# Performance work log

Hardware: AMD Instinct MI355X
Metric: run time of the kernel (lower is better)

Reference implementation:

```python
import jax, jax.numpy as jnp
import numpy as np

V, H, L, B, T = 50000, 256, 2, 4, 1024


def setup_inputs() -> dict:
    key = jax.random.key(0)
    ks = jax.random.split(key, 8)
    s = 1.0 / np.sqrt(H)
    return {
        "input_ids": jax.random.randint(ks[0], (B, T), 0, V),
        "emb": jax.random.normal(ks[1], (V, H), jnp.float32) * 0.02,
        "Wi": jax.random.normal(ks[2], (L, H, H), jnp.float32) * s,
        "bi": jnp.zeros((L, H), jnp.float32),
        "Wf": jax.random.normal(ks[3], (L, H, H), jnp.float32) * s,
        "bf": jnp.zeros((L, H), jnp.float32),
        "Wg": jax.random.normal(ks[4], (L, H, H), jnp.float32) * s,
        "bg": jnp.zeros((L, H), jnp.float32),
        "Wo": jax.random.normal(ks[5], (L, H, H), jnp.float32) * s,
        "bo": jnp.zeros((L, H), jnp.float32),
        "Wp": jax.random.normal(ks[6], (H, V), jnp.float32) * s,
        "bp": jnp.zeros((V,), jnp.float32),
    }


def _hgrn_layer(x, Wi_l, bi_l, Wf_l, bf_l, Wg_l, bg_l, Wo_l, bo_l, lower):
    # x: [B, T, H]
    i = jax.nn.silu(x @ Wi_l + bi_l)                              # input branch
    f = lower + (1.0 - lower) * jax.nn.sigmoid(x @ Wf_l + bf_l)   # bounded forget gate
    g = jax.nn.sigmoid(x @ Wg_l + bg_l)                           # output gate

    def step(h, fi):
        f_t, i_t = fi
        h = f_t * h + (1.0 - f_t) * i_t
        return h, h

    # scan over time: [T, B, H]
    h0 = jnp.zeros_like(x[:, 0])
    h_last, h_seq = jax.lax.scan(step, h0, (jnp.swapaxes(f, 0, 1), jnp.swapaxes(i, 0, 1)))
    h_seq = jnp.swapaxes(h_seq, 0, 1)                             # [B, T, H]
    out = (h_seq * g) @ Wo_l + bo_l
    return x + out, h_last


def reference(input_ids, emb, Wi, bi, Wf, bf, Wg, bg, Wo, bo, Wp, bp):
    x = emb[input_ids]                                            # [B, T, H]
    n_layers = Wi.shape[0]
    hiddens = []
    for l in range(n_layers):
        lower = l / n_layers
        x, h_last = _hgrn_layer(x, Wi[l], bi[l], Wf[l], bf[l], Wg[l], bg[l], Wo[l], bo[l], lower)
        hiddens.append(h_last)
    logits = x @ Wp + bp                                          # [B, T, V]
    return logits, jnp.stack(hiddens)                             # hidden: [L, B, H]
```

## Files before the change

### kernel.cpp

```cpp
#include <hip/hip_runtime.h>


#define VV 50000
#define HH 256
#define LL 2
#define BB 4
#define TT 1024
#define MM 4096
#define HID_OFF 204800000

typedef __attribute__((ext_vector_type(8))) short short8_t;
typedef __attribute__((ext_vector_type(4))) short short4_t;
typedef __attribute__((ext_vector_type(4))) float f32x4_t;

static __device__ __forceinline__ short f2bf(float f) {
  union { float f; unsigned u; } a;
  a.f = f;
  unsigned u = a.u;
  unsigned r = u + 0x7fffu + ((u >> 16) & 1u);
  return (short)(r >> 16);
}

__global__ __launch_bounds__(256) void k_embed(const int* __restrict__ ids,
                                               const float* __restrict__ emb,
                                               float* __restrict__ x,
                                               short* __restrict__ xb) {
  int row = blockIdx.x;
  int h = threadIdx.x;
  int id = ids[row];
  float v = emb[(size_t)id * HH + h];
  x[(size_t)row * HH + h] = v;
  xb[(size_t)row * HH + h] = f2bf(v);
}

__global__ __launch_bounds__(256) void kL1(const short* __restrict__ xb,
                                           const float* __restrict__ Wi,
                                           const float* __restrict__ Wf,
                                           const float* __restrict__ Wg,
                                           const float* __restrict__ bi,
                                           const float* __restrict__ bfv,
                                           const float* __restrict__ bg,
                                           float* __restrict__ gall,
                                           float* __restrict__ P,
                                           float* __restrict__ S,
                                           float lower) {
  __shared__ __align__(16) short Alds[64][264];
  __shared__ __align__(16) short Wlds[64][264];
  __shared__ __align__(16) float Ilds[64][68];
  __shared__ __align__(16) float Flds[64][68];
  __shared__ __align__(16) float bsh3[192];

  int tid = threadIdx.x;
  int mt = blockIdx.x, nt = blockIdx.y;
  int m0 = mt * 64, n0 = nt * 64;

#pragma unroll
  for (int p = 0; p < 8; p++) {
    int idx = p * 256 + tid;
    int row = idx >> 5, ck = idx & 31;
    *(short8_t*)&Alds[row][ck * 8] =
        *(const short8_t*)(xb + (size_t)(m0 + row) * HH + ck * 8);
  }
  if (tid < 64) bsh3[tid] = bi[n0 + tid];
  else if (tid < 128) bsh3[tid] = bfv[n0 + tid - 64];
  else if (tid < 192) bsh3[tid] = bg[n0 + tid - 128];

  int lane = tid & 63, w = tid >> 6, wm = w >> 1, wn = w & 1;
  int r16 = lane & 15, kg = (lane >> 4) * 8;
  int cg = tid & 15, kr = tid >> 4;

  for (int gz = 0; gz < 3; gz++) {
    const float* W = (gz == 0) ? Wi : (gz == 1) ? Wf : Wg;
    float* dst = gall + (size_t)gz * (MM * HH);

    __syncthreads();
#pragma unroll
    for (int p = 0; p < 16; p++) {
      int k = p * 16 + kr;
      float4 wv = *(const float4*)(W + (size_t)k * HH + n0 + cg * 4);
      Wlds[cg * 4 + 0][k] = f2bf(wv.x);
      Wlds[cg * 4 + 1][k] = f2bf(wv.y);
      Wlds[cg * 4 + 2][k] = f2bf(wv.z);
      Wlds[cg * 4 + 3][k] = f2bf(wv.w);
    }
    __syncthreads();

    f32x4_t acc[2][2] = {{{0.f,0.f,0.f,0.f},{0.f,0.f,0.f,0.f}},
                         {{0.f,0.f,0.f,0.f},{0.f,0.f,0.f,0.f}}};
#pragma unroll
    for (int kk = 0; kk < 8; kk++) {
      short8_t w0 = *(const short8_t*)&Wlds[wn * 32 + r16][kk * 32 + kg];
      short8_t w1 = *(const short8_t*)&Wlds[wn * 32 + 16 + r16][kk * 32 + kg];
      short8_t t0 = *(const short8_t*)&Alds[wm * 32 + r16][kk * 32 + kg];
      short8_t t1 = *(const short8_t*)&Alds[wm * 32 + 16 + r16][kk * 32 + kg];
      acc[0][0] = __builtin_amdgcn_mfma_f32_16x16x32_bf16(w0, t0, acc[0][0], 0, 0, 0);
      acc[0][1] = __builtin_amdgcn_mfma_f32_16x16x32_bf16(w0, t1, acc[0][1], 0, 0, 0);
      acc[1][0] = __builtin_amdgcn_mfma_f32_16x16x32_bf16(w1, t0, acc[1][0], 0, 0, 0);
      acc[1][1] = __builtin_amdgcn_mfma_f32_16x16x32_bf16(w1, t1, acc[1][1], 0, 0, 0);
    }
#pragma unroll
    for (int fv = 0; fv < 2; fv++)
#pragma unroll
      for (int ft = 0; ft < 2; ft++) {
        int tl = wm * 32 + ft * 16 + r16;
        int colb = wn * 32 + fv * 16 + (lane >> 4) * 4;
        f32x4_t z4 = acc[fv][ft] + *(const f32x4_t*)&bsh3[gz * 64 + colb];
        f32x4_t a4;
#pragma unroll
        for (int r = 0; r < 4; r++) {
          float z = z4[r];
          if (gz == 0) {
            a4[r] = z / (1.f + __expf(-z));
          } else if (gz == 1) {
            a4[r] = lower + (1.f - lower) / (1.f + __expf(-z));
          } else {
            a4[r] = 1.f / (1.f + __expf(-z));
          }
        }
        *(f32x4_t*)&dst[(size_t)(m0 + tl) * HH + n0 + colb] = a4;
        if (gz == 0) *(f32x4_t*)&Ilds[tl][colb] = a4;
        else if (gz == 1) *(f32x4_t*)&Flds[tl][colb] = a4;
      }
  }
  __syncthreads();

  if (tid < 128) {
    int chunk = tid >> 6, hl = tid & 63;
    float p = 1.f, s = 0.f;
#pragma unroll
    for (int t = 0; t < 32; t++) {
      float fv = Flds[chunk * 32 + t][hl];
      float iv = Ilds[chunk * 32 + t][hl];
      s = fv * s + (1.f - fv) * iv;
      p *= fv;
    }
    int b = mt >> 4;
    int c = (mt & 15) * 2 + chunk;
    int idx = (b * 32 + c) * HH + n0 + hl;
    P[idx] = p;
    S[idx] = s;
  }
}

__global__ __launch_bounds__(256) void k_scan23(const float* __restrict__ gall,
                                                const float* __restrict__ P,
                                                const float* __restrict__ S,
                                                short* __restrict__ hgb,
                                                float* __restrict__ hid,
                                                int l) {
  int bc = blockIdx.x;
  int b = bc >> 5, c = bc & 31;
  int h = threadIdx.x;
  float hv = 0.f;
  for (int cc = 0; cc < c; cc++) {
    int idx = (b * 32 + cc) * HH + h;
    hv = P[idx] * hv + S[idx];
  }
  const float* iptr = gall;
  const float* fptr = gall + (size_t)MM * HH;
  const float* gptr = gall + (size_t)2 * MM * HH;
  size_t base = (size_t)(b * TT + c * 32) * HH + h;
#pragma unroll 8
  for (int t = 0; t < 32; t++) {
    float fv = fptr[base + (size_t)t * HH];
    float iv = iptr[base + (size_t)t * HH];
    float gv = gptr[base + (size_t)t * HH];
    hv = fv * hv + (1.f - fv) * iv;
    hgb[base + (size_t)t * HH] = f2bf(hv * gv);
  }
  if (c == 31) hid[(size_t)(l * BB + b) * HH + h] = hv;
}

__global__ __launch_bounds__(256) void k_wo(const short* __restrict__ hgb,
                                            const float* __restrict__ W,
                                            const float* __restrict__ bias,
                                            float* __restrict__ x,
                                            short* __restrict__ xb) {
  __shared__ __align__(16) short Alds[64][264];
  __shared__ __align__(16) short Wlds[64][264];
  __shared__ __align__(16) float bsh[64];

  int tid = threadIdx.x;
  int m0 = blockIdx.x * 64, n0 = blockIdx.y * 64;

  int cg = tid & 15, kr = tid >> 4;
#pragma unroll
  for (int p = 0; p < 16; p++) {
    int k = p * 16 + kr;
    float4 wv = *(const float4*)(W + (size_t)k * HH + n0 + cg * 4);
    Wlds[cg * 4 + 0][k] = f2bf(wv.x);
    Wlds[cg * 4 + 1][k] = f2bf(wv.y);
    Wlds[cg * 4 + 2][k] = f2bf(wv.z);
    Wlds[cg * 4 + 3][k] = f2bf(wv.w);
  }
  if (tid < 64) bsh[tid] = bias[n0 + tid];
#pragma unroll
  for (int p = 0; p < 8; p++) {
    int idx = p * 256 + tid;
    int row = idx >> 5, ck = idx & 31;
    *(short8_t*)&Alds[row][ck * 8] =
        *(const short8_t*)(hgb + (size_t)(m0 + row) * HH + ck * 8);
  }
  __syncthreads();

  int lane = tid & 63, w = tid >> 6, wm = w >> 1, wn = w & 1;
  int r16 = lane & 15, kg = (lane >> 4) * 8;
  f32x4_t acc[2][2] = {{{0.f,0.f,0.f,0.f},{0.f,0.f,0.f,0.f}},
                       {{0.f,0.f,0.f,0.f},{0.f,0.f,0.f,0.f}}};
#pragma unroll
  for (int kk = 0; kk < 8; kk++) {
    short8_t w0 = *(const short8_t*)&Wlds[wn * 32 + r16][kk * 32 + kg];
    short8_t w1 = *(const short8_t*)&Wlds[wn * 32 + 16 + r16][kk * 32 + kg];
    short8_t t0 = *(const short8_t*)&Alds[wm * 32 + r16][kk * 32 + kg];
    short8_t t1 = *(const short8_t*)&Alds[wm * 32 + 16 + r16][kk * 32 + kg];
    acc[0][0] = __builtin_amdgcn_mfma_f32_16x16x32_bf16(w0, t0, acc[0][0], 0, 0, 0);
    acc[0][1] = __builtin_amdgcn_mfma_f32_16x16x32_bf16(w0, t1, acc[0][1], 0, 0, 0);
    acc[1][0] = __builtin_amdgcn_mfma_f32_16x16x32_bf16(w1, t0, acc[1][0], 0, 0, 0);
    acc[1][1] = __builtin_amdgcn_mfma_f32_16x16x32_bf16(w1, t1, acc[1][1], 0, 0, 0);
  }
#pragma unroll
  for (int fv = 0; fv < 2; fv++)
#pragma unroll
    for (int ft = 0; ft < 2; ft++) {
      int token = m0 + wm * 32 + ft * 16 + r16;
      int colb = wn * 32 + fv * 16 + (lane >> 4) * 4;
      size_t idx = (size_t)token * HH + n0 + colb;
      f32x4_t xv = *(const f32x4_t*)&x[idx];
      xv += acc[fv][ft] + *(const f32x4_t*)&bsh[colb];
      *(f32x4_t*)&x[idx] = xv;
      short4_t xb4;
#pragma unroll
      for (int r = 0; r < 4; r++) xb4[r] = f2bf(xv[r]);
      *(short4_t*)&xb[idx] = xb4;
    }
}

__global__ __launch_bounds__(512) void k_proj(const short* __restrict__ xb,
                                              const float* __restrict__ Wp,
                                              const float* __restrict__ bp,
                                              float* __restrict__ out) {
  __shared__ __align__(16) short Alds[64][264];
  __shared__ __align__(16) float Ost[64][260];
  __shared__ __align__(16) float bsh[256];

  short (*Wst)[264] = (short(*)[264])&Ost[0][0];

  int tid = threadIdx.x;
  int n0 = blockIdx.x * 256;

  int lane = tid & 63, w = tid >> 6;
  int wm = w >> 2, wq = w & 3;
  int r16 = lane & 15, kg = (lane >> 4) * 8;
  int cg = tid & 15, kr = tid >> 4;

  if (tid < 256) bsh[tid] = (n0 + tid < VV) ? bp[n0 + tid] : 0.f;

  short8_t wf[8][4];
  for (int s = 0; s < 4; s++) {
    int c0 = n0 + s * 64;
    bool fullslab = (c0 + 64 <= VV);
#pragma unroll
    for (int p = 0; p < 8; p++) {
      int k = p * 32 + kr;
      if (fullslab) {
        float4 wv = *(const float4*)(Wp + (size_t)k * VV + c0 + cg * 4);
        Wst[cg * 4 + 0][k] = f2bf(wv.x);
        Wst[cg * 4 + 1][k] = f2bf(wv.y);
        Wst[cg * 4 + 2][k] = f2bf(wv.z);
        Wst[cg * 4 + 3][k] = f2bf(wv.w);
      } else {
        for (int j = 0; j < 4; j++) {
          int n = c0 + cg * 4 + j;
          float v = (n < VV) ? Wp[(size_t)k * VV + n] : 0.f;
          Wst[cg * 4 + j][k] = f2bf(v);
        }
      }
    }
    __syncthreads();
    if (wq == s) {
#pragma unroll
      for (int kk = 0; kk < 8; kk++)
#pragma unroll
        for (int cf = 0; cf < 4; cf++)
          wf[kk][cf] = *(const short8_t*)&Wst[cf * 16 + r16][kk * 32 + kg];
    }
    asm volatile("s_waitcnt lgkmcnt(0)" ::: "memory");
    __syncthreads();
  }

  int arow = tid >> 5;
  int ack = tid & 31;

  const int NMT = 32;
  int mbase = blockIdx.y * NMT * 64;

  short8_t areg[4];
#pragma unroll
  for (int p = 0; p < 4; p++)
    areg[p] = *(const short8_t*)(xb + (size_t)(mbase + p * 16 + arow) * HH + ack * 8);

  for (int mi = 0; mi < NMT; mi++) {
    int m0 = mbase + mi * 64;

    __builtin_amdgcn_sched_barrier(0);
    __builtin_amdgcn_s_barrier();
    __builtin_amdgcn_sched_barrier(0);

#pragma unroll
    for (int p = 0; p < 4; p++)
      *(short8_t*)&Alds[p * 16 + arow][ack * 8] = areg[p];

    asm volatile("s_waitcnt lgkmcnt(0)" ::: "memory");
    __builtin_amdgcn_sched_barrier(0);
    __builtin_amdgcn_s_barrier();
    __builtin_amdgcn_sched_barrier(0);

    if (mi + 1 < NMT) {
      int m1 = m0 + 64;
#pragma unroll
      for (int p = 0; p < 4; p++)
        areg[p] = *(const short8_t*)(xb + (size_t)(m1 + p * 16 + arow) * HH + ack * 8);
    }

    f32x4_t acc[2][4] = {{{0.f,0.f,0.f,0.f},{0.f,0.f,0.f,0.f},
                          {0.f,0.f,0.f,0.f},{0.f,0.f,0.f,0.f}},
                         {{0.f,0.f,0.f,0.f},{0.f,0.f,0.f,0.f},
                          {0.f,0.f,0.f,0.f},{0.f,0.f,0.f,0.f}}};
#pragma unroll
    for (int kk = 0; kk < 8; kk++) {
      short8_t t0 = *(const short8_t*)&Alds[wm * 32 + r16][kk * 32 + kg];
      short8_t t1 = *(const short8_t*)&Alds[wm * 32 + 16 + r16][kk * 32 + kg];
#pragma unroll
      for (int cf = 0; cf < 4; cf++) {
        acc[0][cf] = __builtin_amdgcn_mfma_f32_16x16x32_bf16(wf[kk][cf], t0, acc[0][cf], 0, 0, 0);
        acc[1][cf] = __builtin_amdgcn_mfma_f32_16x16x32_bf16(wf[kk][cf], t1, acc[1][cf], 0, 0, 0);
      }
    }

#pragma unroll
    for (int ft = 0; ft < 2; ft++)
#pragma unroll
      for (int cf = 0; cf < 4; cf++) {
        int tok = wm * 32 + ft * 16 + r16;
        int col = wq * 64 + cf * 16 + (lane >> 4) * 4;
        *(f32x4_t*)&Ost[tok][col] = acc[ft][cf];
      }
    asm volatile("s_waitcnt lgkmcnt(0)" ::: "memory");
    __builtin_amdgcn_sched_barrier(0);
    __builtin_amdgcn_s_barrier();
    __builtin_amdgcn_sched_barrier(0);

    int colc = lane * 4;
    bool colok = (n0 + colc < VV);
#pragma unroll
    for (int r = 0; r < 8; r++) {
      int row = w * 8 + r;
      f32x4_t v = *(const f32x4_t*)&Ost[row][colc] + *(const f32x4_t*)&bsh[colc];
      if (colok)
        __builtin_nontemporal_store(v,
            (f32x4_t*)(out + (size_t)(m0 + row) * VV + n0 + colc));
    }
  }
}

extern "C" void kernel_launch(void* const* d_in, const int* in_sizes, int n_in,
                              void* d_out, int out_size, void* d_ws, size_t ws_size,
                              hipStream_t stream) {
  const int* ids = (const int*)d_in[0];
  const float* emb = (const float*)d_in[1];
  const float* Wi = (const float*)d_in[2];
  const float* bi = (const float*)d_in[3];
  const float* Wf = (const float*)d_in[4];
  const float* bfv = (const float*)d_in[5];
  const float* Wg = (const float*)d_in[6];
  const float* bg = (const float*)d_in[7];
  const float* Wo = (const float*)d_in[8];
  const float* bo = (const float*)d_in[9];
  const float* Wp = (const float*)d_in[10];
  const float* bp = (const float*)d_in[11];
  float* out = (float*)d_out;

  char* w = (char*)d_ws;
  float* x = (float*)(w);
  short* xb = (short*)(w + (4u << 20));
  float* gall = (float*)(w + (6u << 20));
  short* hgb = (short*)(w + (18u << 20));
  float* Parr = (float*)(w + (20u << 20));
  float* Sarr = (float*)(w + (20u << 20) + (128u << 10));
  float* hid = out + HID_OFF;

  k_embed<<<MM, 256, 0, stream>>>(ids, emb, x, xb);

  for (int l = 0; l < LL; l++) {
    float lower = (float)l / (float)LL;
    kL1<<<dim3(64, 4), 256, 0, stream>>>(
        xb, Wi + (size_t)l * HH * HH, Wf + (size_t)l * HH * HH,
        Wg + (size_t)l * HH * HH, bi + l * HH, bfv + l * HH, bg + l * HH,
        gall, Parr, Sarr, lower);
    k_scan23<<<BB * 32, 256, 0, stream>>>(gall, Parr, Sarr, hgb, hid, l);
    k_wo<<<dim3(64, 4), 256, 0, stream>>>(hgb, Wo + (size_t)l * HH * HH,
                                          bo + l * HH, x, xb);
  }

  k_proj<<<dim3(196, 2), 512, 0, stream>>>(xb, Wp, bp, out);
}
```

Baseline: 260.1 us.

## Balance projection GEMM work with a flat job list split across 512 blocks

The vocab projection kernel now splits (column-strip, row-tile) jobs evenly across a fixed 512-block grid instead of using a 196x2 grid. The old grid had 392 blocks of 32 row tiles each, which fills the 256 CUs unevenly. Each block processes a contiguous range of about 24-25 jobs and reloads the Wp strip into registers only when its strip index changes. Strip reloads are now serialized inside the job loop, so blocks whose range crosses a strip boundary pay an extra weight-conversion pass.

```diff
diff --git a/kernel.cpp b/kernel.cpp
--- a/kernel.cpp
+++ b/kernel.cpp
@@ -8,6 +8,9 @@
 #define TT 1024
 #define MM 4096
 #define HID_OFF 204800000
+#define NST 196
+#define NJOBS (NST * 64)
+#define NBLK 512
 
 typedef __attribute__((ext_vector_type(8))) short short8_t;
 typedef __attribute__((ext_vector_type(4))) short short4_t;
@@ -246,65 +249,72 @@
   short (*Wst)[264] = (short(*)[264])&Ost[0][0];
 
   int tid = threadIdx.x;
-  int n0 = blockIdx.x * 256;
+  int bid = blockIdx.x;
+  int job0 = (NJOBS * bid) >> 9;
+  int job1 = (NJOBS * (bid + 1)) >> 9;
 
   int lane = tid & 63, w = tid >> 6;
   int wm = w >> 2, wq = w & 3;
   int r16 = lane & 15, kg = (lane >> 4) * 8;
   int cg = tid & 15, kr = tid >> 4;
-
-  if (tid < 256) bsh[tid] = (n0 + tid < VV) ? bp[n0 + tid] : 0.f;
-
-  short8_t wf[8][4];
-  for (int s = 0; s < 4; s++) {
-    int c0 = n0 + s * 64;
-    bool fullslab = (c0 + 64 <= VV);
-#pragma unroll
-    for (int p = 0; p < 8; p++) {
-      int k = p * 32 + kr;
-      if (fullslab) {
-        float4 wv = *(const float4*)(Wp + (size_t)k * VV + c0 + cg * 4);
-        Wst[cg * 4 + 0][k] = f2bf(wv.x);
-        Wst[cg * 4 + 1][k] = f2bf(wv.y);
-        Wst[cg * 4 + 2][k] = f2bf(wv.z);
-        Wst[cg * 4 + 3][k] = f2bf(wv.w);
-      } else {
-        for (int j = 0; j < 4; j++) {
-          int n = c0 + cg * 4 + j;
-          float v = (n < VV) ? Wp[(size_t)k * VV + n] : 0.f;
-          Wst[cg * 4 + j][k] = f2bf(v);
-        }
-      }
-    }
-    __syncthreads();
-    if (wq == s) {
-#pragma unroll
-      for (int kk = 0; kk < 8; kk++)
-#pragma unroll
-        for (int cf = 0; cf < 4; cf++)
-          wf[kk][cf] = *(const short8_t*)&Wst[cf * 16 + r16][kk * 32 + kg];
-    }
-    asm volatile("s_waitcnt lgkmcnt(0)" ::: "memory");
-    __syncthreads();
-  }
-
   int arow = tid >> 5;
   int ack = tid & 31;
 
-  const int NMT = 32;
-  int mbase = blockIdx.y * NMT * 64;
-
+  int cur_st = -1;
+  short8_t wf[8][4];
   short8_t areg[4];
-#pragma unroll
-  for (int p = 0; p < 4; p++)
-    areg[p] = *(const short8_t*)(xb + (size_t)(mbase + p * 16 + arow) * HH + ack * 8);
-
-  for (int mi = 0; mi < NMT; mi++) {
-    int m0 = mbase + mi * 64;
+
+  {
+    int m0 = (job0 & 63) * 64;
+#pragma unroll
+    for (int p = 0; p < 4; p++)
+      areg[p] = *(const short8_t*)(xb + (size_t)(m0 + p * 16 + arow) * HH + ack * 8);
+  }
+
+  for (int job = job0; job < job1; job++) {
+    int st = job >> 6;
+    int m0 = (job & 63) * 64;
+    int n0 = st * 256;
 
     __builtin_amdgcn_sched_barrier(0);
     __builtin_amdgcn_s_barrier();
     __builtin_amdgcn_sched_barrier(0);
+
+    if (st != cur_st) {
+      cur_st = st;
+      if (tid < 256) bsh[tid] = (n0 + tid < VV) ? bp[n0 + tid] : 0.f;
+      for (int s = 0; s < 4; s++) {
+        int c0 = n0 + s * 64;
+        bool fullslab = (c0 + 64 <= VV);
+#pragma unroll
+        for (int p = 0; p < 8; p++) {
+          int k = p * 32 + kr;
+          if (fullslab) {
+            float4 wv = *(const float4*)(Wp + (size_t)k * VV + c0 + cg * 4);
+            Wst[cg * 4 + 0][k] = f2bf(wv.x);
+            Wst[cg * 4 + 1][k] = f2bf(wv.y);
+            Wst[cg * 4 + 2][k] = f2bf(wv.z);
+            Wst[cg * 4 + 3][k] = f2bf(wv.w);
+          } else {
+            for (int j = 0; j < 4; j++) {
+              int n = c0 + cg * 4 + j;
+              float v = (n < VV) ? Wp[(size_t)k * VV + n] : 0.f;
+              Wst[cg * 4 + j][k] = f2bf(v);
+            }
+          }
+        }
+        __syncthreads();
+        if (wq == s) {
+#pragma unroll
+          for (int kk = 0; kk < 8; kk++)
+#pragma unroll
+            for (int cf = 0; cf < 4; cf++)
+              wf[kk][cf] = *(const short8_t*)&Wst[cf * 16 + r16][kk * 32 + kg];
+        }
+        asm volatile("s_waitcnt lgkmcnt(0)" ::: "memory");
+        __syncthreads();
+      }
+    }
 
 #pragma unroll
     for (int p = 0; p < 4; p++)
@@ -315,8 +325,8 @@
     __builtin_amdgcn_s_barrier();
     __builtin_amdgcn_sched_barrier(0);
 
-    if (mi + 1 < NMT) {
-      int m1 = m0 + 64;
+    if (job + 1 < job1) {
+      int m1 = ((job + 1) & 63) * 64;
 #pragma unroll
       for (int p = 0; p < 4; p++)
         areg[p] = *(const short8_t*)(xb + (size_t)(m1 + p * 16 + arow) * HH + ack * 8);
@@ -402,5 +412,5 @@
                                           bo + l * HH, x, xb);
   }
 
-  k_proj<<<dim3(196, 2), 512, 0, stream>>>(xb, Wp, bp, out);
-}
+  k_proj<<<NBLK, 512, 0, stream>>>(xb, Wp, bp, out);
+}
```

Result: slower. 287.2 us (+10.4%).

## Fuse embedding gather into first gate GEMM, split scan blocks, defer projection stores

Applied to the files above, without the earlier changes.

Removes the separate embedding kernel: the layer-0 gate kernel gathers embedding rows directly, converts them to bf16 into LDS, and each column tile writes its slice of the fp32 residual. The scan kernel now runs 256 blocks of 128 threads instead of 128 blocks of 256, so more CUs get work. In the output projection, the store of each tile's logits is moved to the next iteration, after the next A tile is written to LDS, removing one barrier per iteration so the global stores overlap with the next tile's MFMA work. The cost is a redundant embedding gather across the four column-tile blocks and a more intricate LDS reuse ordering in the projection loop.

```diff
diff --git a/kernel.cpp b/kernel.cpp
--- a/kernel.cpp
+++ b/kernel.cpp
@@ -21,19 +21,10 @@
   return (short)(r >> 16);
 }
 
-__global__ __launch_bounds__(256) void k_embed(const int* __restrict__ ids,
-                                               const float* __restrict__ emb,
-                                               float* __restrict__ x,
-                                               short* __restrict__ xb) {
-  int row = blockIdx.x;
-  int h = threadIdx.x;
-  int id = ids[row];
-  float v = emb[(size_t)id * HH + h];
-  x[(size_t)row * HH + h] = v;
-  xb[(size_t)row * HH + h] = f2bf(v);
-}
-
 __global__ __launch_bounds__(256) void kL1(const short* __restrict__ xb,
+                                           const int* __restrict__ ids,
+                                           const float* __restrict__ emb,
+                                           float* __restrict__ x,
                                            const float* __restrict__ Wi,
                                            const float* __restrict__ Wf,
                                            const float* __restrict__ Wg,
@@ -43,7 +34,7 @@
                                            float* __restrict__ gall,
                                            float* __restrict__ P,
                                            float* __restrict__ S,
-                                           float lower) {
+                                           float lower, int layer0) {
   __shared__ __align__(16) short Alds[64][264];
   __shared__ __align__(16) short Wlds[64][264];
   __shared__ __align__(16) float Ilds[64][68];
@@ -54,12 +45,31 @@
   int mt = blockIdx.x, nt = blockIdx.y;
   int m0 = mt * 64, n0 = nt * 64;
 
-#pragma unroll
-  for (int p = 0; p < 8; p++) {
-    int idx = p * 256 + tid;
-    int row = idx >> 5, ck = idx & 31;
-    *(short8_t*)&Alds[row][ck * 8] =
-        *(const short8_t*)(xb + (size_t)(m0 + row) * HH + ck * 8);
+  if (layer0) {
+#pragma unroll
+    for (int p = 0; p < 8; p++) {
+      int idx = p * 256 + tid;
+      int row = idx >> 5, ck = idx & 31;
+      int id = ids[m0 + row];
+      float4 e0 = *(const float4*)(emb + (size_t)id * HH + ck * 8);
+      float4 e1 = *(const float4*)(emb + (size_t)id * HH + ck * 8 + 4);
+      short8_t a8;
+      a8[0] = f2bf(e0.x); a8[1] = f2bf(e0.y); a8[2] = f2bf(e0.z); a8[3] = f2bf(e0.w);
+      a8[4] = f2bf(e1.x); a8[5] = f2bf(e1.y); a8[6] = f2bf(e1.z); a8[7] = f2bf(e1.w);
+      *(short8_t*)&Alds[row][ck * 8] = a8;
+      if ((ck >> 3) == nt) {
+        *(float4*)(x + (size_t)(m0 + row) * HH + ck * 8) = e0;
+        *(float4*)(x + (size_t)(m0 + row) * HH + ck * 8 + 4) = e1;
+      }
+    }
+  } else {
+#pragma unroll
+    for (int p = 0; p < 8; p++) {
+      int idx = p * 256 + tid;
+      int row = idx >> 5, ck = idx & 31;
+      *(short8_t*)&Alds[row][ck * 8] =
+          *(const short8_t*)(xb + (size_t)(m0 + row) * HH + ck * 8);
+    }
   }
   if (tid < 64) bsh3[tid] = bi[n0 + tid];
   else if (tid < 128) bsh3[tid] = bfv[n0 + tid - 64];
@@ -142,15 +152,15 @@
   }
 }
 
-__global__ __launch_bounds__(256) void k_scan23(const float* __restrict__ gall,
+__global__ __launch_bounds__(128) void k_scan23(const float* __restrict__ gall,
                                                 const float* __restrict__ P,
                                                 const float* __restrict__ S,
                                                 short* __restrict__ hgb,
                                                 float* __restrict__ hid,
                                                 int l) {
-  int bc = blockIdx.x;
-  int b = bc >> 5, c = bc & 31;
-  int h = threadIdx.x;
+  int bid = blockIdx.x;
+  int b = bid >> 6, c = (bid >> 1) & 31, half = bid & 1;
+  int h = half * 128 + threadIdx.x;
   float hv = 0.f;
   for (int cc = 0; cc < c; cc++) {
     int idx = (b * 32 + cc) * HH + h;
@@ -290,6 +300,8 @@
 
   int arow = tid >> 5;
   int ack = tid & 31;
+  int colc = lane * 4;
+  bool colok = (n0 + colc < VV);
 
   const int NMT = 32;
   int mbase = blockIdx.y * NMT * 64;
@@ -299,16 +311,24 @@
   for (int p = 0; p < 4; p++)
     areg[p] = *(const short8_t*)(xb + (size_t)(mbase + p * 16 + arow) * HH + ack * 8);
 
+  int m_prev = -1;
   for (int mi = 0; mi < NMT; mi++) {
     int m0 = mbase + mi * 64;
 
-    __builtin_amdgcn_sched_barrier(0);
-    __builtin_amdgcn_s_barrier();
-    __builtin_amdgcn_sched_barrier(0);
-
 #pragma unroll
     for (int p = 0; p < 4; p++)
       *(short8_t*)&Alds[p * 16 + arow][ack * 8] = areg[p];
+
+    if (m_prev >= 0) {
+#pragma unroll
+      for (int r = 0; r < 8; r++) {
+        int row = w * 8 + r;
+        f32x4_t v = *(const f32x4_t*)&Ost[row][colc] + *(const f32x4_t*)&bsh[colc];
+        if (colok)
+          __builtin_nontemporal_store(v,
+              (f32x4_t*)(out + (size_t)(m_prev + row) * VV + n0 + colc));
+      }
+    }
 
     asm volatile("s_waitcnt lgkmcnt(0)" ::: "memory");
     __builtin_amdgcn_sched_barrier(0);
@@ -336,7 +356,6 @@
         acc[1][cf] = __builtin_amdgcn_mfma_f32_16x16x32_bf16(wf[kk][cf], t1, acc[1][cf], 0, 0, 0);
       }
     }
-
 #pragma unroll
     for (int ft = 0; ft < 2; ft++)
 #pragma unroll
@@ -345,21 +364,22 @@
         int col = wq * 64 + cf * 16 + (lane >> 4) * 4;
         *(f32x4_t*)&Ost[tok][col] = acc[ft][cf];
       }
+
     asm volatile("s_waitcnt lgkmcnt(0)" ::: "memory");
     __builtin_amdgcn_sched_barrier(0);
     __builtin_amdgcn_s_barrier();
     __builtin_amdgcn_sched_barrier(0);
 
-    int colc = lane * 4;
-    bool colok = (n0 + colc < VV);
-#pragma unroll
-    for (int r = 0; r < 8; r++) {
-      int row = w * 8 + r;
-      f32x4_t v = *(const f32x4_t*)&Ost[row][colc] + *(const f32x4_t*)&bsh[colc];
-      if (colok)
-        __builtin_nontemporal_store(v,
-            (f32x4_t*)(out + (size_t)(m0 + row) * VV + n0 + colc));
-    }
+    m_prev = m0;
+  }
+
+#pragma unroll
+  for (int r = 0; r < 8; r++) {
+    int row = w * 8 + r;
+    f32x4_t v = *(const f32x4_t*)&Ost[row][colc] + *(const f32x4_t*)&bsh[colc];
+    if (colok)
+      __builtin_nontemporal_store(v,
+          (f32x4_t*)(out + (size_t)(m_prev + row) * VV + n0 + colc));
   }
 }
 
@@ -389,15 +409,14 @@
   float* Sarr = (float*)(w + (20u << 20) + (128u << 10));
   float* hid = out + HID_OFF;
 
-  k_embed<<<MM, 256, 0, stream>>>(ids, emb, x, xb);
-
   for (int l = 0; l < LL; l++) {
     float lower = (float)l / (float)LL;
     kL1<<<dim3(64, 4), 256, 0, stream>>>(
-        xb, Wi + (size_t)l * HH * HH, Wf + (size_t)l * HH * HH,
+        xb, ids, emb, x,
+        Wi + (size_t)l * HH * HH, Wf + (size_t)l * HH * HH,
         Wg + (size_t)l * HH * HH, bi + l * HH, bfv + l * HH, bg + l * HH,
-        gall, Parr, Sarr, lower);
-    k_scan23<<<BB * 32, 256, 0, stream>>>(gall, Parr, Sarr, hgb, hid, l);
+        gall, Parr, Sarr, lower, l == 0 ? 1 : 0);
+    k_scan23<<<256, 128, 0, stream>>>(gall, Parr, Sarr, hgb, hid, l);
     k_wo<<<dim3(64, 4), 256, 0, stream>>>(hgb, Wo + (size_t)l * HH * HH,
                                           bo + l * HH, x, xb);
   }
```

After: 265.2 us. About the same (+2.0%).
